# Optimization experiments

Measured on AMD Instinct MI355X. Metric: run time of the kernel, lower is better.

Reference implementation:

```python
import jax, jax.numpy as jnp
import numpy as np
from jax import lax

EPS = 1e-06
K = 7  # kernel_size
C1 = 0.01 ** 2
C2 = 0.03 ** 2

_SOBEL_X = jnp.array([[-1.0, 0.0, 1.0], [-2.0, 0.0, 2.0], [-1.0, 0.0, 1.0]], dtype=jnp.float32).reshape(1, 1, 3, 3)
_SOBEL_Y = jnp.array([[-1.0, -2.0, -1.0], [0.0, 0.0, 0.0], [1.0, 2.0, 1.0]], dtype=jnp.float32).reshape(1, 1, 3, 3)


def _conv3x3(x, w):
    # NCHW cross-correlation with zero padding=1 (matches F.conv2d)
    return lax.conv_general_dilated(
        x, w, window_strides=(1, 1), padding=[(1, 1), (1, 1)],
        dimension_numbers=('NCHW', 'OIHW', 'NCHW'))


def _box(x):
    # avg_pool2d(k, stride=1, pad=k//2, count_include_pad=True):
    # sum over zero-padded window, divide by k*k everywhere.
    p = K // 2
    s = lax.reduce_window(x, jnp.float32(0.0), lax.add,
                          window_dimensions=(1, 1, K, K),
                          window_strides=(1, 1, 1, 1),
                          padding=[(0, 0), (0, 0), (p, p), (p, p)])
    return s / jnp.float32(K * K)


def _grad_mag(x):
    gx = _conv3x3(x, _SOBEL_X)
    gy = _conv3x3(x, _SOBEL_Y)
    return jnp.sqrt(gx * gx + gy * gy + EPS)


def setup_inputs() -> dict:
    key = jax.random.key(0)
    k1, k2 = jax.random.split(key)
    B, H, W = 64, 512, 512
    pred = jax.random.normal(k1, (B, 1, H, W), dtype=jnp.float32)
    target = jax.random.normal(k2, (B, 1, H, W), dtype=jnp.float32)
    min_target = jnp.zeros((B,), dtype=jnp.float32)
    max_target = jnp.ones((B,), dtype=jnp.float32)
    return {"pred": pred, "target": target, "min_target": min_target, "max_target": max_target}


def reference(pred, target, min_target, max_target):
    B = pred.shape[0]
    mn = min_target.reshape(B, 1, 1, 1)
    mx = max_target.reshape(B, 1, 1, 1)
    dr = jnp.maximum(mx - mn, EPS)
    p = (pred - mn) / dr
    t = (target - mn) / dr

    gp = _grad_mag(p)
    gt = _grad_mag(t)

    mu_p = _box(p)
    mu_t = _box(t)
    luminance = (2.0 * mu_p * mu_t + C1) / (mu_p * mu_p + mu_t * mu_t + C1)

    mu_gp = _box(gp)
    mu_gt = _box(gt)
    sig_p = _box(gp * gp) - mu_gp * mu_gp
    sig_t = _box(gt * gt) - mu_gt * mu_gt
    sig_x = _box(gp * gt) - mu_gp * mu_gt
    cs = (2.0 * sig_x + C2) / (sig_p + sig_t + C2)

    return 1.0 - jnp.mean(luminance * cs)
```

## Files before the change

kernel.cpp:

```cpp
#include <hip/hip_runtime.h>
#include <hip/hip_fp16.h>
#include <math.h>


constexpr int NT = 256;
constexpr float EPS_F = 1e-6f;
constexpr float C1S = 2401.0f * 0.0001f;
constexpr float C2S = 2401.0f * 0.0009f;

union U4 { uint4 u; __half2 h[4]; };
union F4U { float4 v; float a[4]; };

__device__ __forceinline__ __half2 h2swap(__half2 x) {
    unsigned u = __builtin_bit_cast(unsigned, x);
    u = (u >> 16) | (u << 16);
    return __builtin_bit_cast(__half2, u);
}

__device__ __forceinline__ float ssim_px(__half2 apt, __half2 ag, __half2 agg, __half2 agx) {
    float2 vpt = __half22float2(apt);
    float2 vg  = __half22float2(ag);
    float2 vgg = __half22float2(agg);
    float  vgx = __low2float(agx);
    float lum_n = 2.0f * vpt.x * vpt.y + C1S;
    float lum_d = vpt.x * vpt.x + vpt.y * vpt.y + C1S;
    float cs_n  = 2.0f * (49.0f * vgx - vg.x * vg.y) + C2S;
    float cs_d  = 49.0f * (vgg.x + vgg.y) - vg.x * vg.x - vg.y * vg.y + C2S;
    return lum_n * cs_n * __builtin_amdgcn_rcpf(lum_d * cs_d);
}

__global__ __launch_bounds__(NT, 4)
void gssim_strip(const float* __restrict__ pred, const float* __restrict__ target,
                 const float* __restrict__ mn_arr, const float* __restrict__ mx_arr,
                 float* __restrict__ partial) {
    constexpr int H = 512, W = 512;
    __shared__ alignas(16) __half2 spt[40][44];
    __shared__ alignas(16) __half2 sg[38][40];
    __shared__ alignas(16) __half2 hsAll[38][32][4];

    const int blk  = blockIdx.x;
    const int b    = blk >> 5;
    const int rem  = blk & 31;
    const int gy0  = (rem >> 1) * 32;
    const int tx0  = (rem & 1) * 8;
    const int tid  = threadIdx.x;

    const float mn     = mn_arr[b];
    const float inv_dr = 1.0f / fmaxf(mx_arr[b] - mn, EPS_F);
    const float* pimg = pred   + (size_t)b * H * W;
    const float* timg = target + (size_t)b * H * W;

    const int gS  = tid % 10;
    const int yr  = tid / 10;
    const int yS0 = 2 * yr, yS1 = yS0 + 1;
    const int gyS0 = gy0 - 4 + yS0;
    const int gyS1 = gyS0 + 1;
    const bool rok0 = (gyS0 >= 0 && gyS0 < H);
    const bool rok1 = (gyS1 >= 0 && gyS1 < H);
    const bool hasS = (tid < 200);

    F4U Pa0, Ta0, Pa1, Ta1;

    auto stage1 = [&](int gx0n, bool rowok, int gyI, F4U& P, F4U& T) {
        int gx = gx0n - 4 + 4 * gS;
        P.v = make_float4(0.f, 0.f, 0.f, 0.f);
        T.v = make_float4(0.f, 0.f, 0.f, 0.f);
        if (rowok) {
            if (gx >= 0 && gx + 4 <= W) {
                P.v = *reinterpret_cast<const float4*>(pimg + (size_t)gyI * W + gx);
                T.v = *reinterpret_cast<const float4*>(timg + (size_t)gyI * W + gx);
            } else {
#pragma unroll
                for (int c = 0; c < 4; ++c) {
                    int x = gx + c;
                    if (x >= 0 && x < W) {
                        P.a[c] = pimg[(size_t)gyI * W + x];
                        T.a[c] = timg[(size_t)gyI * W + x];
                    }
                }
            }
        }
    };
    auto stagePair = [&](int gx0n) {
        stage1(gx0n, rok0, gyS0, Pa0, Ta0);
        stage1(gx0n, rok1, gyS1, Pa1, Ta1);
    };

    auto writeOne = [&](F4U& P, F4U& T, int y, bool rowok, int gx0n) {
        int gx = gx0n - 4 + 4 * gS;
        U4 w;
#pragma unroll
        for (int c = 0; c < 4; ++c) {
            int x = gx + c;
            bool ok = rowok && (x >= 0) && (x < W);
            float pv = ok ? (P.a[c] - mn) * inv_dr : 0.f;
            float tv = ok ? (T.a[c] - mn) * inv_dr : 0.f;
            w.h[c] = __floats2half2_rn(pv, tv);
        }
        *reinterpret_cast<uint4*>(&spt[y][4 * gS]) = w.u;
    };
    auto writePair = [&](int gx0n) {
        writeOne(Pa0, Ta0, yS0, rok0, gx0n);
        writeOne(Pa1, Ta1, yS1, rok1, gx0n);
    };

    const __half2 two2  = __float2half2_rn(2.0f);
    const __half2 eps2  = __float2half2_rn(1e-6f);
    const __half2 zero2 = __float2half2_rn(0.0f);

    if (hasS) { stagePair(tx0 * 32); writePair(tx0 * 32); }
    __syncthreads();

    float accl = 0.0f;

    for (int tt = 0; tt < 8; ++tt) {
        const int gx0 = (tx0 + tt) * 32;

        if (tt < 7 && hasS) stagePair(gx0 + 32);

        if (tid < 190) {
            const int g  = tid % 10, kr = tid / 10;
            const int j0 = 4 * g, k0 = 2 * kr;
            __half2 a[4][6];
#pragma unroll
            for (int r = 0; r < 4; ++r) {
                U4 v; v.u = *reinterpret_cast<const uint4*>(&spt[k0 + r][j0]);
                a[r][0] = v.h[0]; a[r][1] = v.h[1]; a[r][2] = v.h[2]; a[r][3] = v.h[3];
                uint2 v2 = *reinterpret_cast<const uint2*>(&spt[k0 + r][j0 + 4]);
                a[r][4] = __builtin_bit_cast(__half2, v2.x);
                a[r][5] = __builtin_bit_cast(__half2, v2.y);
            }
            bool cm[4];
#pragma unroll
            for (int c = 0; c < 4; ++c) {
                int gc = gx0 + j0 + c - 3;
                cm[c] = (gc >= 0 && gc < W);
            }
#pragma unroll
            for (int rr = 0; rr < 2; ++rr) {
                const int k = k0 + rr;
                const int gr = gy0 + k - 3;
                U4 w; w.h[0] = zero2; w.h[1] = zero2; w.h[2] = zero2; w.h[3] = zero2;
                if (gr >= 0 && gr < H) {
#pragma unroll
                    for (int c = 0; c < 4; ++c) {
                        __half2 gxh = __hsub2(a[rr][c + 2], a[rr][c]);
                        gxh = __hfma2(two2, __hsub2(a[rr + 1][c + 2], a[rr + 1][c]), gxh);
                        gxh = __hadd2(gxh, __hsub2(a[rr + 2][c + 2], a[rr + 2][c]));
                        __half2 gyh = __hsub2(a[rr + 2][c], a[rr][c]);
                        gyh = __hfma2(two2, __hsub2(a[rr + 2][c + 1], a[rr][c + 1]), gyh);
                        gyh = __hadd2(gyh, __hsub2(a[rr + 2][c + 2], a[rr][c + 2]));
                        __half2 m2 = __hfma2(gxh, gxh, __hfma2(gyh, gyh, eps2));
                        __half2 mag = h2sqrt(m2);
                        w.h[c] = cm[c] ? mag : zero2;
                    }
                }
                *reinterpret_cast<uint4*>(&sg[k][j0]) = w.u;
            }
        }
        __syncthreads();

        if (tid < 152) {
            const int kr = tid % 19, cg = tid / 19;
            const int c0 = 4 * cg;
#pragma unroll
            for (int rr = 0; rr < 2; ++rr) {
                const int k = kr + 19 * rr;
                __half2 ptv[12], sgv[12];
#pragma unroll
                for (int q = 0; q < 3; ++q) {
                    U4 v; v.u = *reinterpret_cast<const uint4*>(&spt[k + 1][c0 + 4 * q]);
                    ptv[4 * q] = v.h[0]; ptv[4 * q + 1] = v.h[1]; ptv[4 * q + 2] = v.h[2]; ptv[4 * q + 3] = v.h[3];
                    U4 u; u.u = *reinterpret_cast<const uint4*>(&sg[k][c0 + 4 * q]);
                    sgv[4 * q] = u.h[0]; sgv[4 * q + 1] = u.h[1]; sgv[4 * q + 2] = u.h[2]; sgv[4 * q + 3] = u.h[3];
                }
                __half2 gg[10], gx2[10];
#pragma unroll
                for (int q = 0; q < 10; ++q) {
                    gg[q]  = __hmul2(sgv[q], sgv[q]);
                    gx2[q] = __hmul2(sgv[q], h2swap(sgv[q]));
                }
                __half2 Hpt = ptv[1], Hg = sgv[0], Hgg = gg[0], Hgx = gx2[0];
#pragma unroll
                for (int q = 1; q < 7; ++q) {
                    Hpt = __hadd2(Hpt, ptv[q + 1]);
                    Hg  = __hadd2(Hg,  sgv[q]);
                    Hgg = __hadd2(Hgg, gg[q]);
                    Hgx = __hadd2(Hgx, gx2[q]);
                }
                U4 w0;
                w0.h[0] = Hpt; w0.h[1] = Hg; w0.h[2] = Hgg; w0.h[3] = Hgx;
                *reinterpret_cast<uint4*>(&hsAll[k][(c0 + k) & 31][0]) = w0.u;
#pragma unroll
                for (int m = 1; m < 4; ++m) {
                    Hpt = __hadd2(__hsub2(Hpt, ptv[m]),      ptv[m + 7]);
                    Hg  = __hadd2(__hsub2(Hg,  sgv[m - 1]),  sgv[m + 6]);
                    Hgg = __hadd2(__hsub2(Hgg, gg[m - 1]),   gg[m + 6]);
                    Hgx = __hadd2(__hsub2(Hgx, gx2[m - 1]),  gx2[m + 6]);
                    U4 w;
                    w.h[0] = Hpt; w.h[1] = Hg; w.h[2] = Hgg; w.h[3] = Hgx;
                    *reinterpret_cast<uint4*>(&hsAll[k][(c0 + m + k) & 31][0]) = w.u;
                }
            }
        }
        __syncthreads();

        {
            const int ox = tid & 31;
            const int q  = tid >> 5;
            const int r0 = 4 * q;
            U4 win[10];
#pragma unroll
            for (int j = 0; j < 7; ++j) {
                int r = r0 + j;
                win[j].u = *reinterpret_cast<const uint4*>(&hsAll[r][(ox + r) & 31][0]);
            }
            __half2 Spt = win[0].h[0], Sg = win[0].h[1], Sgg = win[0].h[2], Sgx = win[0].h[3];
#pragma unroll
            for (int j = 1; j < 7; ++j) {
                Spt = __hadd2(Spt, win[j].h[0]);
                Sg  = __hadd2(Sg,  win[j].h[1]);
                Sgg = __hadd2(Sgg, win[j].h[2]);
                Sgx = __hadd2(Sgx, win[j].h[3]);
            }
            accl += ssim_px(Spt, Sg, Sgg, Sgx);
#pragma unroll
            for (int s = 1; s < 4; ++s) {
                int r = r0 + 6 + s;
                win[6 + s].u = *reinterpret_cast<const uint4*>(&hsAll[r][(ox + r) & 31][0]);
                Spt = __hadd2(__hsub2(Spt, win[s - 1].h[0]), win[6 + s].h[0]);
                Sg  = __hadd2(__hsub2(Sg,  win[s - 1].h[1]), win[6 + s].h[1]);
                Sgg = __hadd2(__hsub2(Sgg, win[s - 1].h[2]), win[6 + s].h[2]);
                Sgx = __hadd2(__hsub2(Sgx, win[s - 1].h[3]), win[6 + s].h[3]);
                accl += ssim_px(Spt, Sg, Sgg, Sgx);
            }
        }

        if (tt < 7 && hasS) writePair(gx0 + 32);
        __syncthreads();
    }

    float* red = reinterpret_cast<float*>(&spt[0][0]);
#pragma unroll
    for (int off = 32; off > 0; off >>= 1) accl += __shfl_down(accl, off, 64);
    if ((tid & 63) == 0) red[tid >> 6] = accl;
    __syncthreads();
    if (tid == 0) partial[blk] = red[0] + red[1] + red[2] + red[3];
}

__global__ __launch_bounds__(256)
void gssim_final(const float* __restrict__ partial, int n,
                 float* __restrict__ out, double inv_count) {
    __shared__ double sred[256];
    double acc = 0.0;
    for (int i = threadIdx.x; i < n; i += 256) acc += (double)partial[i];
    sred[threadIdx.x] = acc;
    __syncthreads();
    for (int s = 128; s > 0; s >>= 1) {
        if ((int)threadIdx.x < s) sred[threadIdx.x] += sred[threadIdx.x + s];
        __syncthreads();
    }
    if (threadIdx.x == 0) out[0] = (float)(1.0 - sred[0] * inv_count);
}

extern "C" void kernel_launch(void* const* d_in, const int* in_sizes, int n_in,
                              void* d_out, int out_size, void* d_ws, size_t ws_size,
                              hipStream_t stream) {
    const float* pred   = (const float*)d_in[0];
    const float* target = (const float*)d_in[1];
    const float* mn     = (const float*)d_in[2];
    const float* mx     = (const float*)d_in[3];
    float* out = (float*)d_out;

    const int B = in_sizes[2];
    const int H = 512, W = 512;

    float* partial = (float*)d_ws;

    const int nblocks = B * (H / 32) * 2;
    gssim_strip<<<nblocks, NT, 0, stream>>>(pred, target, mn, mx, partial);

    const double inv_count = 1.0 / ((double)B * (double)H * (double)W);
    gssim_final<<<1, 256, 0, stream>>>(partial, nblocks, out, inv_count);
}
```

Baseline: 75.68 us.

## Add interior fast paths and rebalance horizontal box-sum work across threads

Adds interior-tile fast paths that skip per-element boundary checks in global staging and in the Sobel gradient stage. Normalization moves to packed half2 arithmetic instead of per-float math. The horizontal-sum phase is redistributed from 152 threads doing two rows each to 304 single-row units across all 256 threads, which shortens the critical path between barriers. This grows code size and slightly changes normalization precision, since the subtract and scale now happen in fp16.

```diff
diff --git a/kernel.cpp b/kernel.cpp
--- a/kernel.cpp
+++ b/kernel.cpp
@@ -47,8 +47,12 @@
 
     const float mn     = mn_arr[b];
     const float inv_dr = 1.0f / fmaxf(mx_arr[b] - mn, EPS_F);
+    const __half2 mn2  = __float2half2_rn(mn);
+    const __half2 inv2 = __float2half2_rn(inv_dr);
     const float* pimg = pred   + (size_t)b * H * W;
     const float* timg = target + (size_t)b * H * W;
+
+    const bool rows_ok_all = (gy0 >= 4) && (gy0 + 35 < H);
 
     const int gS  = tid % 10;
     const int yr  = tid / 10;
@@ -61,7 +65,7 @@
 
     F4U Pa0, Ta0, Pa1, Ta1;
 
-    auto stage1 = [&](int gx0n, bool rowok, int gyI, F4U& P, F4U& T) {
+    auto stage1m = [&](int gx0n, bool rowok, int gyI, F4U& P, F4U& T) {
         int gx = gx0n - 4 + 4 * gS;
         P.v = make_float4(0.f, 0.f, 0.f, 0.f);
         T.v = make_float4(0.f, 0.f, 0.f, 0.f);
@@ -82,26 +86,42 @@
         }
     };
     auto stagePair = [&](int gx0n) {
-        stage1(gx0n, rok0, gyS0, Pa0, Ta0);
-        stage1(gx0n, rok1, gyS1, Pa1, Ta1);
+        if (rows_ok_all && gx0n >= 4 && gx0n <= 448) {
+            int gx = gx0n - 4 + 4 * gS;
+            Pa0.v = *reinterpret_cast<const float4*>(pimg + (size_t)gyS0 * W + gx);
+            Ta0.v = *reinterpret_cast<const float4*>(timg + (size_t)gyS0 * W + gx);
+            Pa1.v = *reinterpret_cast<const float4*>(pimg + (size_t)gyS1 * W + gx);
+            Ta1.v = *reinterpret_cast<const float4*>(timg + (size_t)gyS1 * W + gx);
+        } else {
+            stage1m(gx0n, rok0, gyS0, Pa0, Ta0);
+            stage1m(gx0n, rok1, gyS1, Pa1, Ta1);
+        }
     };
 
-    auto writeOne = [&](F4U& P, F4U& T, int y, bool rowok, int gx0n) {
-        int gx = gx0n - 4 + 4 * gS;
-        U4 w;
-#pragma unroll
-        for (int c = 0; c < 4; ++c) {
-            int x = gx + c;
-            bool ok = rowok && (x >= 0) && (x < W);
-            float pv = ok ? (P.a[c] - mn) * inv_dr : 0.f;
-            float tv = ok ? (T.a[c] - mn) * inv_dr : 0.f;
-            w.h[c] = __floats2half2_rn(pv, tv);
-        }
-        *reinterpret_cast<uint4*>(&spt[y][4 * gS]) = w.u;
+    auto normh2 = [&](float p, float t) {
+        return __hmul2(__hsub2(__floats2half2_rn(p, t), mn2), inv2);
     };
     auto writePair = [&](int gx0n) {
-        writeOne(Pa0, Ta0, yS0, rok0, gx0n);
-        writeOne(Pa1, Ta1, yS1, rok1, gx0n);
+        U4 w0, w1;
+        if (rows_ok_all && gx0n >= 4 && gx0n <= 448) {
+#pragma unroll
+            for (int c = 0; c < 4; ++c) {
+                w0.h[c] = normh2(Pa0.a[c], Ta0.a[c]);
+                w1.h[c] = normh2(Pa1.a[c], Ta1.a[c]);
+            }
+        } else {
+            int gx = gx0n - 4 + 4 * gS;
+            const __half2 zero2l = __float2half2_rn(0.0f);
+#pragma unroll
+            for (int c = 0; c < 4; ++c) {
+                int x = gx + c;
+                bool okc = (x >= 0) && (x < W);
+                w0.h[c] = (rok0 && okc) ? normh2(Pa0.a[c], Ta0.a[c]) : zero2l;
+                w1.h[c] = (rok1 && okc) ? normh2(Pa1.a[c], Ta1.a[c]) : zero2l;
+            }
+        }
+        *reinterpret_cast<uint4*>(&spt[yS0][4 * gS]) = w0.u;
+        *reinterpret_cast<uint4*>(&spt[yS1][4 * gS]) = w1.u;
     };
 
     const __half2 two2  = __float2half2_rn(2.0f);
@@ -115,6 +135,7 @@
 
     for (int tt = 0; tt < 8; ++tt) {
         const int gx0 = (tx0 + tt) * 32;
+        const bool interior = rows_ok_all && (gx0 >= 32) && (gx0 <= 448);
 
         if (tt < 7 && hasS) stagePair(gx0 + 32);
 
@@ -130,18 +151,11 @@
                 a[r][4] = __builtin_bit_cast(__half2, v2.x);
                 a[r][5] = __builtin_bit_cast(__half2, v2.y);
             }
-            bool cm[4];
-#pragma unroll
-            for (int c = 0; c < 4; ++c) {
-                int gc = gx0 + j0 + c - 3;
-                cm[c] = (gc >= 0 && gc < W);
-            }
-#pragma unroll
-            for (int rr = 0; rr < 2; ++rr) {
-                const int k = k0 + rr;
-                const int gr = gy0 + k - 3;
-                U4 w; w.h[0] = zero2; w.h[1] = zero2; w.h[2] = zero2; w.h[3] = zero2;
-                if (gr >= 0 && gr < H) {
+            if (interior) {
+#pragma unroll
+                for (int rr = 0; rr < 2; ++rr) {
+                    const int k = k0 + rr;
+                    U4 w;
 #pragma unroll
                     for (int c = 0; c < 4; ++c) {
                         __half2 gxh = __hsub2(a[rr][c + 2], a[rr][c]);
@@ -150,59 +164,83 @@
                         __half2 gyh = __hsub2(a[rr + 2][c], a[rr][c]);
                         gyh = __hfma2(two2, __hsub2(a[rr + 2][c + 1], a[rr][c + 1]), gyh);
                         gyh = __hadd2(gyh, __hsub2(a[rr + 2][c + 2], a[rr][c + 2]));
-                        __half2 m2 = __hfma2(gxh, gxh, __hfma2(gyh, gyh, eps2));
-                        __half2 mag = h2sqrt(m2);
-                        w.h[c] = cm[c] ? mag : zero2;
+                        w.h[c] = h2sqrt(__hfma2(gxh, gxh, __hfma2(gyh, gyh, eps2)));
                     }
+                    *reinterpret_cast<uint4*>(&sg[k][j0]) = w.u;
                 }
-                *reinterpret_cast<uint4*>(&sg[k][j0]) = w.u;
+            } else {
+                bool cm[4];
+#pragma unroll
+                for (int c = 0; c < 4; ++c) {
+                    int gc = gx0 + j0 + c - 3;
+                    cm[c] = (gc >= 0 && gc < W);
+                }
+#pragma unroll
+                for (int rr = 0; rr < 2; ++rr) {
+                    const int k = k0 + rr;
+                    const int gr = gy0 + k - 3;
+                    U4 w; w.h[0] = zero2; w.h[1] = zero2; w.h[2] = zero2; w.h[3] = zero2;
+                    if (gr >= 0 && gr < H) {
+#pragma unroll
+                        for (int c = 0; c < 4; ++c) {
+                            __half2 gxh = __hsub2(a[rr][c + 2], a[rr][c]);
+                            gxh = __hfma2(two2, __hsub2(a[rr + 1][c + 2], a[rr + 1][c]), gxh);
+                            gxh = __hadd2(gxh, __hsub2(a[rr + 2][c + 2], a[rr + 2][c]));
+                            __half2 gyh = __hsub2(a[rr + 2][c], a[rr][c]);
+                            gyh = __hfma2(two2, __hsub2(a[rr + 2][c + 1], a[rr][c + 1]), gyh);
+                            gyh = __hadd2(gyh, __hsub2(a[rr + 2][c + 2], a[rr][c + 2]));
+                            __half2 mag = h2sqrt(__hfma2(gxh, gxh, __hfma2(gyh, gyh, eps2)));
+                            w.h[c] = cm[c] ? mag : zero2;
+                        }
+                    }
+                    *reinterpret_cast<uint4*>(&sg[k][j0]) = w.u;
+                }
             }
         }
         __syncthreads();
 
-        if (tid < 152) {
-            const int kr = tid % 19, cg = tid / 19;
+        auto p3unit = [&](int t) {
+            const int cg = t / 38;
+            const int k  = t - cg * 38;
             const int c0 = 4 * cg;
-#pragma unroll
-            for (int rr = 0; rr < 2; ++rr) {
-                const int k = kr + 19 * rr;
-                __half2 ptv[12], sgv[12];
-#pragma unroll
-                for (int q = 0; q < 3; ++q) {
-                    U4 v; v.u = *reinterpret_cast<const uint4*>(&spt[k + 1][c0 + 4 * q]);
-                    ptv[4 * q] = v.h[0]; ptv[4 * q + 1] = v.h[1]; ptv[4 * q + 2] = v.h[2]; ptv[4 * q + 3] = v.h[3];
-                    U4 u; u.u = *reinterpret_cast<const uint4*>(&sg[k][c0 + 4 * q]);
-                    sgv[4 * q] = u.h[0]; sgv[4 * q + 1] = u.h[1]; sgv[4 * q + 2] = u.h[2]; sgv[4 * q + 3] = u.h[3];
-                }
-                __half2 gg[10], gx2[10];
-#pragma unroll
-                for (int q = 0; q < 10; ++q) {
-                    gg[q]  = __hmul2(sgv[q], sgv[q]);
-                    gx2[q] = __hmul2(sgv[q], h2swap(sgv[q]));
-                }
-                __half2 Hpt = ptv[1], Hg = sgv[0], Hgg = gg[0], Hgx = gx2[0];
-#pragma unroll
-                for (int q = 1; q < 7; ++q) {
-                    Hpt = __hadd2(Hpt, ptv[q + 1]);
-                    Hg  = __hadd2(Hg,  sgv[q]);
-                    Hgg = __hadd2(Hgg, gg[q]);
-                    Hgx = __hadd2(Hgx, gx2[q]);
-                }
-                U4 w0;
-                w0.h[0] = Hpt; w0.h[1] = Hg; w0.h[2] = Hgg; w0.h[3] = Hgx;
-                *reinterpret_cast<uint4*>(&hsAll[k][(c0 + k) & 31][0]) = w0.u;
-#pragma unroll
-                for (int m = 1; m < 4; ++m) {
-                    Hpt = __hadd2(__hsub2(Hpt, ptv[m]),      ptv[m + 7]);
-                    Hg  = __hadd2(__hsub2(Hg,  sgv[m - 1]),  sgv[m + 6]);
-                    Hgg = __hadd2(__hsub2(Hgg, gg[m - 1]),   gg[m + 6]);
-                    Hgx = __hadd2(__hsub2(Hgx, gx2[m - 1]),  gx2[m + 6]);
-                    U4 w;
-                    w.h[0] = Hpt; w.h[1] = Hg; w.h[2] = Hgg; w.h[3] = Hgx;
-                    *reinterpret_cast<uint4*>(&hsAll[k][(c0 + m + k) & 31][0]) = w.u;
-                }
-            }
-        }
+            __half2 ptv[12], sgv[12];
+#pragma unroll
+            for (int q = 0; q < 3; ++q) {
+                U4 v; v.u = *reinterpret_cast<const uint4*>(&spt[k + 1][c0 + 4 * q]);
+                ptv[4 * q] = v.h[0]; ptv[4 * q + 1] = v.h[1]; ptv[4 * q + 2] = v.h[2]; ptv[4 * q + 3] = v.h[3];
+                U4 u; u.u = *reinterpret_cast<const uint4*>(&sg[k][c0 + 4 * q]);
+                sgv[4 * q] = u.h[0]; sgv[4 * q + 1] = u.h[1]; sgv[4 * q + 2] = u.h[2]; sgv[4 * q + 3] = u.h[3];
+            }
+            __half2 gg[10], gx2[10];
+#pragma unroll
+            for (int q = 0; q < 10; ++q) {
+                gg[q]  = __hmul2(sgv[q], sgv[q]);
+                gx2[q] = __hmul2(sgv[q], h2swap(sgv[q]));
+            }
+            __half2 Hpt = ptv[1], Hg = sgv[0], Hgg = gg[0], Hgx = gx2[0];
+#pragma unroll
+            for (int q = 1; q < 7; ++q) {
+                Hpt = __hadd2(Hpt, ptv[q + 1]);
+                Hg  = __hadd2(Hg,  sgv[q]);
+                Hgg = __hadd2(Hgg, gg[q]);
+                Hgx = __hadd2(Hgx, gx2[q]);
+            }
+            U4 w0;
+            w0.h[0] = Hpt; w0.h[1] = Hg; w0.h[2] = Hgg; w0.h[3] = Hgx;
+            *reinterpret_cast<uint4*>(&hsAll[k][(c0 + k) & 31][0]) = w0.u;
+#pragma unroll
+            for (int m = 1; m < 4; ++m) {
+                Hpt = __hadd2(__hsub2(Hpt, ptv[m]),      ptv[m + 7]);
+                Hg  = __hadd2(__hsub2(Hg,  sgv[m - 1]),  sgv[m + 6]);
+                Hgg = __hadd2(__hsub2(Hgg, gg[m - 1]),   gg[m + 6]);
+                Hgx = __hadd2(__hsub2(Hgx, gx2[m - 1]),  gx2[m + 6]);
+                U4 w;
+                w.h[0] = Hpt; w.h[1] = Hg; w.h[2] = Hgg; w.h[3] = Hgx;
+                *reinterpret_cast<uint4*>(&hsAll[k][(c0 + m + k) & 31][0]) = w.u;
+            }
+        };
+        p3unit(tid);
+        if (tid < 48) p3unit(tid + 256);
         __syncthreads();
 
         {
```

Result: faster. 71.43 us (median of 3 runs) (-5.6%).
